# Kernel optimization log

Hardware: AMD Instinct MI355X
Metric: run time of the kernel (lower is better)

## Reference

```python
import jax, jax.numpy as jnp
import numpy as np

B, C, L, D, E, K = 64, 23, 26000, 64, 512, 3  # batch, chromosomes, bins/chr, d_model, eos_dim, num_states
V = C * L


def setup_inputs() -> dict:
    key = jax.random.key(0)
    k0, k1, k2, k3 = jax.random.split(key, 4)
    return {
        "eos_emb": jax.random.normal(k0, (B, C, E), jnp.float32),
        "bin_ids": jnp.arange(C * L, dtype=jnp.int32).reshape(C, L),
        "emb_table": jax.random.normal(k1, (V, D), jnp.float32) * 0.02,
        "eos_W": jax.random.normal(k2, (D, E), jnp.float32) / np.float32(np.sqrt(E)),
        "eos_b": jnp.zeros((D,), jnp.float32),
        "fc_W": jax.random.normal(k3, (K, 2 * D), jnp.float32) / np.float32(np.sqrt(2 * D)),
        "fc_b": jnp.zeros((K,), jnp.float32),
    }


def reference(eos_emb, bin_ids, emb_table, eos_W, eos_b, fc_W, fc_b):
    # eos_projection (use_eos_proj=True): [B,C,E] @ [D,E]^T + b -> [B,C,D]
    eos = jnp.einsum('bce,de->bcd', eos_emb, eos_W) + eos_b
    # per-chromosome embedding gather (bin_projection skipped: bin_emb_dim == d_model, use_bin_proj=False)
    bin_emb = emb_table[bin_ids]  # [C,L,D]
    # fc on concat([bin, eos]) == bin @ Wb^T + eos @ We^T + b (avoids materializing [B,C,L,2D])
    Wb, We = fc_W[:, :D], fc_W[:, D:]
    a = jnp.einsum('cld,kd->clk', bin_emb, Wb)          # [C,L,K]
    e = jnp.einsum('bcd,kd->bck', eos, We) + fc_b       # [B,C,K]
    return jax.nn.relu(a[None, :, :, :] + e[:, :, None, :])  # [B,C,L,K]
```

## Files before the change

### kernel.cpp

```cpp
#include <hip/hip_runtime.h>

#define NB 64
#define NC 23
#define NL 26000
#define ND 64
#define NE 512
#define NK 3
#define NCL (NC * NL)
#define FP4 (NL * NK / 4)
#define BSTRIDE4 ((size_t)NC * FP4)

typedef float v4f __attribute__((ext_vector_type(4)));

__global__ __launch_bounds__(256) void eos_e_kernel(
    const float* __restrict__ eos_emb,
    const float* __restrict__ eos_W,
    const float* __restrict__ eos_b,
    const float* __restrict__ fc_W,
    const float* __restrict__ fc_b,
    float* __restrict__ e_out)
{
    const int bc = blockIdx.x;
    const int t  = threadIdx.x;
    const int q  = t & 3;
    const int d  = t >> 2;

    __shared__ v4f xs4[NE / 4];
    if (t < NE / 4)
        xs4[t] = reinterpret_cast<const v4f*>(eos_emb + (size_t)bc * NE)[t];
    __syncthreads();

    const v4f* wrow = reinterpret_cast<const v4f*>(eos_W + (size_t)d * NE);
    v4f acc = (v4f)(0.f);
    #pragma unroll 8
    for (int j = 0; j < NE / 16; ++j) {
        const int idx = q + 4 * j;
        acc += wrow[idx] * xs4[idx];
    }
    float p = (acc.x + acc.y) + (acc.z + acc.w);
    p += __shfl_xor(p, 1, 64);
    p += __shfl_xor(p, 2, 64);
    const float eosd = p + eos_b[d];

    __shared__ float part[4][NK];
    #pragma unroll
    for (int k = 0; k < NK; ++k) {
        float pk = eosd * fc_W[k * (2 * ND) + ND + d];
        pk += __shfl_xor(pk,  4, 64);
        pk += __shfl_xor(pk,  8, 64);
        pk += __shfl_xor(pk, 16, 64);
        pk += __shfl_xor(pk, 32, 64);
        if ((t & 63) == 0) part[t >> 6][k] = pk;
    }
    __syncthreads();
    if (t < NK)
        e_out[(size_t)bc * NK + t] =
            part[0][t] + part[1][t] + part[2][t] + part[3][t] + fc_b[t];
}

__global__ __launch_bounds__(256) void a_kernel(
    const int*   __restrict__ bin_ids,
    const float* __restrict__ emb_table,
    const float* __restrict__ fc_W,
    float* __restrict__ a_out)
{
    const int c = blockIdx.y;
    const int t = threadIdx.x;
    const int q = t & 3;
    const int r = t >> 2;
    const int l = blockIdx.x * 64 + r;

    __shared__ v4f wb4[NK][ND / 4];
    if (t < NK * (ND / 4)) {
        const int k = t / (ND / 4), i = t % (ND / 4);
        wb4[k][i] = reinterpret_cast<const v4f*>(fc_W + (size_t)k * (2 * ND))[i];
    }
    __syncthreads();
    if (l >= NL) return;

    const int row = bin_ids[(size_t)c * NL + l];
    const v4f* er = reinterpret_cast<const v4f*>(emb_table + (size_t)row * ND);

    v4f s0 = (v4f)(0.f), s1 = (v4f)(0.f), s2 = (v4f)(0.f);
    #pragma unroll
    for (int j = 0; j < 4; ++j) {
        const int idx = q + 4 * j;
        const v4f v = er[idx];
        s0 += v * wb4[0][idx];
        s1 += v * wb4[1][idx];
        s2 += v * wb4[2][idx];
    }
    float a0 = (s0.x + s0.y) + (s0.z + s0.w);
    float a1 = (s1.x + s1.y) + (s1.z + s1.w);
    float a2 = (s2.x + s2.y) + (s2.z + s2.w);
    a0 += __shfl_xor(a0, 1, 64); a0 += __shfl_xor(a0, 2, 64);
    a1 += __shfl_xor(a1, 1, 64); a1 += __shfl_xor(a1, 2, 64);
    a2 += __shfl_xor(a2, 1, 64); a2 += __shfl_xor(a2, 2, 64);

    if (q < NK) {
        const float val = (q == 0) ? a0 : (q == 1) ? a1 : a2;
        a_out[((size_t)c * NL + l) * NK + q] = val;
    }
}

__global__ __launch_bounds__(256) void bstream_kernel(
    const float* __restrict__ a_in,
    const float* __restrict__ e_in,
    float* __restrict__ out)
{
    const int bx = blockIdx.x;
    const int c  = blockIdx.y;
    const int b0 = blockIdx.z * 16;
    const int t  = threadIdx.x;

    __shared__ v4f e4[3][17];
    if (t < 3 * 16) {
        const int p  = t >> 4;
        const int bl = t & 15;
        const float* ep = e_in + ((size_t)(b0 + bl) * NC + c) * NK;
        const float e0 = ep[0], e1 = ep[1], e2 = ep[2];
        v4f v;
        if      (p == 0) { v.x = e0; v.y = e1; v.z = e2; v.w = e0; }
        else if (p == 1) { v.x = e1; v.y = e2; v.z = e0; v.w = e1; }
        else             { v.x = e2; v.y = e0; v.z = e1; v.w = e2; }
        e4[p][bl] = v;
    }
    __syncthreads();

    const int f0 = bx * 768 + t;
    const int f1 = f0 + 256;
    const int f2 = f0 + 512;
    const bool g0 = f0 < FP4, g1 = f1 < FP4, g2 = f2 < FP4;

    const v4f* a4 = reinterpret_cast<const v4f*>(a_in) + (size_t)c * FP4;
    v4f av0 = (v4f)(0.f), av1 = (v4f)(0.f), av2 = (v4f)(0.f);
    if (g0) av0 = a4[f0];
    if (g1) av1 = a4[f1];
    if (g2) av2 = a4[f2];

    const v4f* ep0 = &e4[f0 % 3][0];
    const v4f* ep1 = &e4[f1 % 3][0];
    const v4f* ep2 = &e4[f2 % 3][0];

    v4f* o4 = reinterpret_cast<v4f*>(out);
    size_t i0 = (size_t)b0 * BSTRIDE4 + (size_t)c * FP4 + f0;
    size_t i1 = i0 + 256;
    size_t i2 = i0 + 512;

    #pragma unroll 4
    for (int bl = 0; bl < 16; ++bl) {
        if (g0) {
            const v4f ev = ep0[bl];
            v4f o;
            o.x = fmaxf(av0.x + ev.x, 0.f);
            o.y = fmaxf(av0.y + ev.y, 0.f);
            o.z = fmaxf(av0.z + ev.z, 0.f);
            o.w = fmaxf(av0.w + ev.w, 0.f);
            o4[i0] = o;
        }
        if (g1) {
            const v4f ev = ep1[bl];
            v4f o;
            o.x = fmaxf(av1.x + ev.x, 0.f);
            o.y = fmaxf(av1.y + ev.y, 0.f);
            o.z = fmaxf(av1.z + ev.z, 0.f);
            o.w = fmaxf(av1.w + ev.w, 0.f);
            o4[i1] = o;
        }
        if (g2) {
            const v4f ev = ep2[bl];
            v4f o;
            o.x = fmaxf(av2.x + ev.x, 0.f);
            o.y = fmaxf(av2.y + ev.y, 0.f);
            o.z = fmaxf(av2.z + ev.z, 0.f);
            o.w = fmaxf(av2.w + ev.w, 0.f);
            o4[i2] = o;
        }
        i0 += BSTRIDE4;
        i1 += BSTRIDE4;
        i2 += BSTRIDE4;
    }
}

__global__ __launch_bounds__(256) void decoder_fused_kernel(
    const int*   __restrict__ bin_ids,
    const float* __restrict__ emb_table,
    const float* __restrict__ fc_W,
    const float* __restrict__ e_in,
    float* __restrict__ out)
{
    const int c   = blockIdx.y;
    const int tid = threadIdx.x;
    const int l   = blockIdx.x * 256 + tid;

    __shared__ float wb[NK][ND];
    __shared__ float es[NB * NK];

    if (tid < NK * ND)
        wb[tid / ND][tid % ND] = fc_W[(tid / ND) * (2 * ND) + (tid % ND)];
    if (tid < NB * NK) {
        int b = tid / NK, k = tid % NK;
        es[tid] = e_in[((size_t)b * NC + c) * NK + k];
    }
    __syncthreads();
    if (l >= NL) return;

    const int row = bin_ids[(size_t)c * NL + l];
    const float4* er = reinterpret_cast<const float4*>(emb_table + (size_t)row * ND);
    const float4* w0 = reinterpret_cast<const float4*>(wb[0]);
    const float4* w1 = reinterpret_cast<const float4*>(wb[1]);
    const float4* w2 = reinterpret_cast<const float4*>(wb[2]);

    float a0 = 0.f, a1 = 0.f, a2 = 0.f;
    #pragma unroll
    for (int i = 0; i < ND / 4; ++i) {
        float4 v  = er[i];
        float4 p0 = w0[i], p1 = w1[i], p2 = w2[i];
        a0 += v.x * p0.x + v.y * p0.y + v.z * p0.z + v.w * p0.w;
        a1 += v.x * p1.x + v.y * p1.y + v.z * p1.z + v.w * p1.w;
        a2 += v.x * p2.x + v.y * p2.y + v.z * p2.z + v.w * p2.w;
    }

    size_t obase = ((size_t)c * NL + l) * NK;
    const size_t bstride = (size_t)NC * NL * NK;
    #pragma unroll 4
    for (int b = 0; b < NB; ++b) {
        const float e0 = es[b * NK + 0];
        const float e1 = es[b * NK + 1];
        const float e2 = es[b * NK + 2];
        out[obase + 0] = fmaxf(a0 + e0, 0.f);
        out[obase + 1] = fmaxf(a1 + e1, 0.f);
        out[obase + 2] = fmaxf(a2 + e2, 0.f);
        obase += bstride;
    }
}

extern "C" void kernel_launch(void* const* d_in, const int* in_sizes, int n_in,
                              void* d_out, int out_size, void* d_ws, size_t ws_size,
                              hipStream_t stream) {
    const float* eos_emb   = (const float*)d_in[0];
    const int*   bin_ids   = (const int*)  d_in[1];
    const float* emb_table = (const float*)d_in[2];
    const float* eos_W     = (const float*)d_in[3];
    const float* eos_b     = (const float*)d_in[4];
    const float* fc_W      = (const float*)d_in[5];
    const float* fc_b      = (const float*)d_in[6];
    float*       out       = (float*)d_out;

    float*  e_ws = (float*)d_ws;
    const size_t a_off_bytes = 32768;
    float*  a_ws = (float*)((char*)d_ws + a_off_bytes);
    const size_t a_bytes = (size_t)NC * NL * NK * sizeof(float);

    eos_e_kernel<<<NB * NC, 256, 0, stream>>>(eos_emb, eos_W, eos_b, fc_W, fc_b, e_ws);

    if (ws_size >= a_off_bytes + a_bytes) {
        dim3 grid_a((NL + 63) / 64, NC);
        a_kernel<<<grid_a, 256, 0, stream>>>(bin_ids, emb_table, fc_W, a_ws);

        dim3 grid_b((FP4 + 767) / 768, NC, 4);
        bstream_kernel<<<grid_b, 256, 0, stream>>>(a_ws, e_ws, out);
    } else {
        dim3 grid((NL + 255) / 256, NC);
        decoder_fused_kernel<<<grid, 256, 0, stream>>>(bin_ids, emb_table, fc_W, e_ws, out);
    }
}
```

Baseline: 147.9 us.

## Flatten broadcast kernel over chromosomes with larger per-block chunks and batch groups

Restructures the broadcast-add-relu stream kernel so each block covers a contiguous 3504-float4 chunk spanning all chromosomes, for 8 batches, instead of a per-chromosome 768-element slice for 16 batches. The e values for all chromosomes are staged in shared memory and indexed per element. The aim is longer contiguous write streams and better load balance across the store-bound output. In exchange it raises register pressure (14 vectors per thread) and adds per-element chromosome index math.

```diff
diff --git a/kernel.cpp b/kernel.cpp
--- a/kernel.cpp
+++ b/kernel.cpp
@@ -6,9 +6,12 @@
 #define ND 64
 #define NE 512
 #define NK 3
-#define NCL (NC * NL)
-#define FP4 (NL * NK / 4)
-#define BSTRIDE4 ((size_t)NC * FP4)
+#define FP4  (NL * NK / 4)
+#define CFP4 (NC * FP4)
+#define CHUNK 3504
+#define NCHUNK 128
+#define NJ 14
+#define GB 8
 
 typedef float v4f __attribute__((ext_vector_type(4)));
 
@@ -109,76 +112,60 @@
     float* __restrict__ out)
 {
     const int bx = blockIdx.x;
-    const int c  = blockIdx.y;
-    const int b0 = blockIdx.z * 16;
+    const int b0 = blockIdx.y * GB;
     const int t  = threadIdx.x;
 
-    __shared__ v4f e4[3][17];
-    if (t < 3 * 16) {
-        const int p  = t >> 4;
-        const int bl = t & 15;
+    __shared__ v4f e4[3][NC][GB];
+    for (int i = t; i < 3 * NC * GB; i += 256) {
+        const int p   = i / (NC * GB);
+        const int rem = i - p * (NC * GB);
+        const int c   = rem / GB;
+        const int bl  = rem - c * GB;
         const float* ep = e_in + ((size_t)(b0 + bl) * NC + c) * NK;
         const float e0 = ep[0], e1 = ep[1], e2 = ep[2];
         v4f v;
         if      (p == 0) { v.x = e0; v.y = e1; v.z = e2; v.w = e0; }
         else if (p == 1) { v.x = e1; v.y = e2; v.z = e0; v.w = e1; }
         else             { v.x = e2; v.y = e0; v.z = e1; v.w = e2; }
-        e4[p][bl] = v;
-    }
-    __syncthreads();
-
-    const int f0 = bx * 768 + t;
-    const int f1 = f0 + 256;
-    const int f2 = f0 + 512;
-    const bool g0 = f0 < FP4, g1 = f1 < FP4, g2 = f2 < FP4;
-
-    const v4f* a4 = reinterpret_cast<const v4f*>(a_in) + (size_t)c * FP4;
-    v4f av0 = (v4f)(0.f), av1 = (v4f)(0.f), av2 = (v4f)(0.f);
-    if (g0) av0 = a4[f0];
-    if (g1) av1 = a4[f1];
-    if (g2) av2 = a4[f2];
-
-    const v4f* ep0 = &e4[f0 % 3][0];
-    const v4f* ep1 = &e4[f1 % 3][0];
-    const v4f* ep2 = &e4[f2 % 3][0];
+        e4[p][c][bl] = v;
+    }
+    __syncthreads();
+
+    const int base = bx * CHUNK;
+    const v4f* a4 = reinterpret_cast<const v4f*>(a_in);
+
+    v4f        av[NJ];
+    const v4f* eptr[NJ];
+    bool       gj[NJ];
+    #pragma unroll
+    for (int j = 0; j < NJ; ++j) {
+        const int fo = j * 256 + t;
+        const int f  = base + fo;
+        gj[j] = (fo < CHUNK) && (f < CFP4);
+        const int fc = gj[j] ? f : 0;
+        const int p  = fc % 3;
+        const int c  = fc / FP4;
+        eptr[j] = &e4[p][c][0];
+        av[j]   = gj[j] ? a4[fc] : (v4f)(0.f);
+    }
 
     v4f* o4 = reinterpret_cast<v4f*>(out);
-    size_t i0 = (size_t)b0 * BSTRIDE4 + (size_t)c * FP4 + f0;
-    size_t i1 = i0 + 256;
-    size_t i2 = i0 + 512;
-
-    #pragma unroll 4
-    for (int bl = 0; bl < 16; ++bl) {
-        if (g0) {
-            const v4f ev = ep0[bl];
-            v4f o;
-            o.x = fmaxf(av0.x + ev.x, 0.f);
-            o.y = fmaxf(av0.y + ev.y, 0.f);
-            o.z = fmaxf(av0.z + ev.z, 0.f);
-            o.w = fmaxf(av0.w + ev.w, 0.f);
-            o4[i0] = o;
+    size_t obase = (size_t)b0 * CFP4 + base;
+    #pragma unroll 2
+    for (int bl = 0; bl < GB; ++bl) {
+        #pragma unroll
+        for (int j = 0; j < NJ; ++j) {
+            if (gj[j]) {
+                const v4f ev = eptr[j][bl];
+                v4f o;
+                o.x = fmaxf(av[j].x + ev.x, 0.f);
+                o.y = fmaxf(av[j].y + ev.y, 0.f);
+                o.z = fmaxf(av[j].z + ev.z, 0.f);
+                o.w = fmaxf(av[j].w + ev.w, 0.f);
+                o4[obase + j * 256 + t] = o;
+            }
         }
-        if (g1) {
-            const v4f ev = ep1[bl];
-            v4f o;
-            o.x = fmaxf(av1.x + ev.x, 0.f);
-            o.y = fmaxf(av1.y + ev.y, 0.f);
-            o.z = fmaxf(av1.z + ev.z, 0.f);
-            o.w = fmaxf(av1.w + ev.w, 0.f);
-            o4[i1] = o;
-        }
-        if (g2) {
-            const v4f ev = ep2[bl];
-            v4f o;
-            o.x = fmaxf(av2.x + ev.x, 0.f);
-            o.y = fmaxf(av2.y + ev.y, 0.f);
-            o.z = fmaxf(av2.z + ev.z, 0.f);
-            o.w = fmaxf(av2.w + ev.w, 0.f);
-            o4[i2] = o;
-        }
-        i0 += BSTRIDE4;
-        i1 += BSTRIDE4;
-        i2 += BSTRIDE4;
+        obase += CFP4;
     }
 }
 
@@ -258,7 +245,7 @@
         dim3 grid_a((NL + 63) / 64, NC);
         a_kernel<<<grid_a, 256, 0, stream>>>(bin_ids, emb_table, fc_W, a_ws);
 
-        dim3 grid_b((FP4 + 767) / 768, NC, 4);
+        dim3 grid_b(NCHUNK, NB / GB);
         bstream_kernel<<<grid_b, 256, 0, stream>>>(a_ws, e_ws, out);
     } else {
         dim3 grid((NL + 255) / 256, NC);
```

Measured after the change: 146.6 us. About the same (-0.9%).
